# Performance work log

Hardware: AMD Instinct MI355X
Metric: run time of the kernel (lower is better)

## Reference

```python
import math
import jax, jax.numpy as jnp
import numpy as np


def setup_inputs() -> dict:
    key = jax.random.key(0)
    k1, k2, k3, k4 = jax.random.split(key, 4)
    B, CK, CV, T, H, W = 4, 64, 512, 8, 30, 30
    mk = jax.random.normal(k1, (B, CK, T, H, W), dtype=jnp.float32)
    qk = jax.random.normal(k2, (B, CK, H, W), dtype=jnp.float32)
    mv = jax.random.normal(k3, (B, CV, T, H, W), dtype=jnp.float32)
    qv = jax.random.normal(k4, (B, CV, H, W), dtype=jnp.float32)
    return {"mk": mk, "qk": qk, "mv": mv, "qv": qv}


def reference(mk, qk, mv, qv):
    # mk: [B, CK, T, H, W], qk: [B, CK, H, W]
    # mv: [B, CV, T, H, W], qv: [B, CV, H, W]
    B, CK, T, H, W = mk.shape
    CV = mv.shape[1]
    mkf = mk.reshape(B, CK, T * H * W)          # [B, CK, THW]
    qkf = qk.reshape(B, CK, H * W)              # [B, CK, HW]
    # distance-based affinity: (2 a.b - |a|^2) / sqrt(CK)
    a_sq = jnp.sum(mkf * mkf, axis=1)[:, :, None]        # [B, THW, 1]
    ab = jnp.einsum('bcm,bcq->bmq', mkf, qkf)            # [B, THW, HW]
    affinity = (2.0 * ab - a_sq) * (1.0 / math.sqrt(CK))
    # softmax over the memory dimension (THW)
    affinity = jax.nn.softmax(affinity, axis=1)          # [B, THW, HW]
    # value readout
    mvf = mv.reshape(B, CV, T * H * W)                   # [B, CV, THW]
    mem = jnp.einsum('bcm,bmq->bcq', mvf, affinity)      # [B, CV, HW]
    mem = mem.reshape(B, CV, H, W)
    return jnp.concatenate([mem, qv], axis=1)            # [B, 2*CV, H, W]
```

## Files before the change

kernel.cpp:

```cpp
#include <hip/hip_runtime.h>

#define B_ 4
#define CK 64
#define CV 512
#define HW_ 900
#define THW 7200
#define MT 96
#define QB 64
#define CVB 128
#define NS 3
#define MSPL (THW / NS)
#define NIT (MSPL / MT)
#define ETP 104

typedef __attribute__((ext_vector_type(4))) float f32x4;
typedef __attribute__((ext_vector_type(4))) float float4_;
typedef __attribute__((ext_vector_type(8))) short s16x8;
typedef __attribute__((ext_vector_type(4))) short s16x4;

__device__ __forceinline__ short f2bf(float f) {
  union { float f; unsigned u; } x; x.f = f;
  unsigned u = x.u;
  return (short)((u + 0x7fffu + ((u >> 16) & 1u)) >> 16);
}

#define NBLK_A 113
#define NBLK_B 900
#define NBLK_C 14400
#define NBLK_D 1800
__global__ __launch_bounds__(256) void prep_kernel(const float* __restrict__ mk,
                                                   const float* __restrict__ qk,
                                                   const float* __restrict__ mv,
                                                   const float* __restrict__ qv,
                                                   short* __restrict__ mkT,
                                                   short* __restrict__ qkb,
                                                   short* __restrict__ mvb,
                                                   float* __restrict__ asq,
                                                   float* __restrict__ out) {
  int bid = blockIdx.x;
  if (bid < NBLK_A) {
    int idx = bid * 256 + threadIdx.x;
    if (idx >= B_ * THW) return;
    int b = idx / THW, m = idx - b * THW;
    const float* src = mk + (size_t)b * CK * THW + m;
    short row[CK];
    float acc = 0.f;
#pragma unroll
    for (int k = 0; k < CK; ++k) {
      float v = src[(size_t)k * THW];
      acc += v * v;
      row[k] = f2bf(v);
    }
    short* dst = mkT + (size_t)idx * CK;
#pragma unroll
    for (int c = 0; c < CK / 8; ++c)
      *reinterpret_cast<s16x8*>(dst + c * 8) = *reinterpret_cast<s16x8*>(row + c * 8);
    asq[idx] = acc * 0.18033688011112042f;
  } else if (bid < NBLK_A + NBLK_B) {
    int i = (bid - NBLK_A) * 256 + threadIdx.x;
    if (i < B_ * CK * HW_) qkb[i] = f2bf(qk[i] * 0.36067376022224085f);
  } else if (bid < NBLK_A + NBLK_B + NBLK_C) {
    int i = (bid - (NBLK_A + NBLK_B)) * 256 + threadIdx.x;
    float4_ v = reinterpret_cast<const float4_*>(mv)[i];
    s16x4 o;
    o[0] = f2bf(v[0]); o[1] = f2bf(v[1]); o[2] = f2bf(v[2]); o[3] = f2bf(v[3]);
    *reinterpret_cast<s16x4*>(mvb + (size_t)i * 4) = o;
  } else {
    int i = (bid - (NBLK_A + NBLK_B + NBLK_C)) * 256 + threadIdx.x;
    const int perb = CV * HW_ / 4;
    int b = i / perb, r = i - b * perb;
    float4_ v = reinterpret_cast<const float4_*>(qv)[i];
    *reinterpret_cast<float4_*>(out + (size_t)b * 2 * CV * HW_ + CV * HW_ + (size_t)r * 4) = v;
  }
}

__global__ __launch_bounds__(256, 4) void attn_kernel(const short* __restrict__ mkT,
                                                      const short* __restrict__ qkb,
                                                      const short* __restrict__ mvb,
                                                      const float* __restrict__ asq,
                                                      float* __restrict__ part,
                                                      float* __restrict__ denomp) {
  __shared__ short e_t[64][ETP];

  const int tid = threadIdx.x;
  const int wave = tid >> 6, lane = tid & 63;
  const int g = lane >> 4, c = lane & 15;
  const int qb = blockIdx.x;
  const int cvc = blockIdx.y & 3, s = blockIdx.y >> 2;
  const int b = blockIdx.z;
  const int q = qb * QB + wave * 16 + c;

  s16x8 qkf[2];
  {
    const short* qs = qkb + (size_t)b * CK * HW_;
#pragma unroll
    for (int ks = 0; ks < 2; ++ks)
#pragma unroll
      for (int j = 0; j < 8; ++j)
        qkf[ks][j] = (q < HW_) ? qs[(size_t)(ks * 32 + g * 8 + j) * HW_ + q] : (short)0;
  }

  f32x4 acc[2][4];
#pragma unroll
  for (int i = 0; i < 2; ++i)
#pragma unroll
    for (int j = 0; j < 4; ++j) acc[i][j] = (f32x4){0.f, 0.f, 0.f, 0.f};
  float denom = 0.f;

  const short* mkb = mkT + (size_t)b * THW * CK;
  const short* mvB = mvb + ((size_t)b * CV + cvc * CVB + wave * 32) * THW;
  const float* asb = asq + (size_t)b * THW;

  for (int it = 0; it < NIT; ++it) {
    const int m0 = s * MSPL + it * MT;

    s16x8 mvf[2][3];
#pragma unroll
    for (int af = 0; af < 2; ++af)
#pragma unroll
      for (int ks = 0; ks < 3; ++ks)
        mvf[af][ks] = *reinterpret_cast<const s16x8*>(
            mvB + (size_t)(af * 16 + c) * THW + m0 + ks * 32 + g * 8);

#pragma unroll
    for (int mf = 0; mf < 6; ++mf) {
      f32x4 sa = (f32x4){0.f, 0.f, 0.f, 0.f};
#pragma unroll
      for (int ks = 0; ks < 2; ++ks) {
        s16x8 a = *reinterpret_cast<const s16x8*>(
            mkb + (size_t)(m0 + mf * 16 + c) * CK + ks * 32 + g * 8);
        sa = __builtin_amdgcn_mfma_f32_16x16x32_bf16(a, qkf[ks], sa, 0, 0, 0);
      }
      f32x4 av = *reinterpret_cast<const f32x4*>(asb + m0 + mf * 16 + g * 4);
      s16x4 e4;
#pragma unroll
      for (int r = 0; r < 4; ++r) {
        float e = exp2f(sa[r] - av[r]);
        denom += e;
        union { float f; unsigned u; } cu; cu.f = e;
        e4[r] = (short)(cu.u >> 16);
      }
      *reinterpret_cast<s16x4*>(&e_t[wave * 16 + c][mf * 16 + g * 4]) = e4;
    }
    __syncthreads();

#pragma unroll
    for (int ks = 0; ks < 3; ++ks) {
      s16x8 ef[4];
#pragma unroll
      for (int qf = 0; qf < 4; ++qf)
        ef[qf] = *reinterpret_cast<const s16x8*>(&e_t[qf * 16 + c][ks * 32 + g * 8]);
#pragma unroll
      for (int af = 0; af < 2; ++af)
#pragma unroll
        for (int qf = 0; qf < 4; ++qf)
          acc[af][qf] =
              __builtin_amdgcn_mfma_f32_16x16x32_bf16(mvf[af][ks], ef[qf], acc[af][qf], 0, 0, 0);
    }
    __syncthreads();
  }

  denom += __shfl_xor(denom, 16);
  denom += __shfl_xor(denom, 32);
  if (cvc == 0 && lane < 16)
    denomp[((size_t)s * B_ + b) * 960 + qb * QB + wave * 16 + lane] = denom;

  float* pb = part + (size_t)(((s * B_ + b) * 4 + cvc) * 15 + qb) * 8192;
#pragma unroll
  for (int af = 0; af < 2; ++af)
#pragma unroll
    for (int qf = 0; qf < 4; ++qf)
#pragma unroll
      for (int r = 0; r < 4; ++r)
        pb[(size_t)(wave * 32 + af * 16 + g * 4 + r) * 64 + qf * 16 + c] = acc[af][qf][r];
}

__global__ __launch_bounds__(256) void finalize_kernel(const float* __restrict__ part,
                                                       const float* __restrict__ denomp,
                                                       float* __restrict__ out) {
  int t = blockIdx.x * 256 + threadIdx.x;
  int q4 = t & 15;
  int cvl = (t >> 4) & 127;
  int r1 = t >> 11;
  int qb = r1 % 15;
  int r2 = r1 / 15;
  int cvc = r2 & 3;
  int b = r2 >> 2;
  int q0 = qb * QB + q4 * 4;
  if (q0 >= HW_) return;
  const size_t sstr = (size_t)B_ * 4 * 15 * 8192;
  size_t base = (size_t)((b * 4 + cvc) * 15 + qb) * 8192 + cvl * 64 + q4 * 4;
  f32x4 p = *reinterpret_cast<const f32x4*>(part + base);
  f32x4 p1 = *reinterpret_cast<const f32x4*>(part + base + sstr);
  f32x4 p2 = *reinterpret_cast<const f32x4*>(part + base + 2 * sstr);
  p = p + p1 + p2;
  const float* dp = denomp + (size_t)b * 960 + q0;
  f32x4 d = *reinterpret_cast<const f32x4*>(dp) +
            *reinterpret_cast<const f32x4*>(dp + B_ * 960) +
            *reinterpret_cast<const f32x4*>(dp + 2 * B_ * 960);
  f32x4 o;
#pragma unroll
  for (int j = 0; j < 4; ++j) o[j] = p[j] / d[j];
  *reinterpret_cast<f32x4*>(out + (size_t)b * 2 * CV * HW_ +
                            (size_t)(cvc * CVB + cvl) * HW_ + q0) = o;
}

extern "C" void kernel_launch(void* const* d_in, const int* in_sizes, int n_in,
                              void* d_out, int out_size, void* d_ws, size_t ws_size,
                              hipStream_t stream) {
  const float* mk = (const float*)d_in[0];
  const float* qk = (const float*)d_in[1];
  const float* mv = (const float*)d_in[2];
  const float* qv = (const float*)d_in[3];
  float* out = (float*)d_out;

  char* ws = (char*)d_ws;
  short* mvb   = (short*)ws;
  short* mkT   = (short*)(ws + 29491200);
  short* qkb   = (short*)(ws + 33177600);
  float* asq   = (float*)(ws + 33638400);
  float* denomp= (float*)(ws + 33753600);
  float* part  = (float*)(ws + 33799680);

  prep_kernel<<<dim3(NBLK_A + NBLK_B + NBLK_C + NBLK_D), dim3(256), 0, stream>>>(
      mk, qk, mv, qv, mkT, qkb, mvb, asq, out);
  attn_kernel<<<dim3(15, 4 * NS, B_), dim3(256), 0, stream>>>(mkT, qkb, mvb, asq, part, denomp);
  finalize_kernel<<<dim3(1920), dim3(256), 0, stream>>>(part, denomp, out);
}
```

Before: 284.6 us.

## Double-buffer mv/mk tiles into LDS via async global_load_lds with swizzling

The attention kernel now stages the value, key and asq tiles for the next memory chunk into double-buffered LDS using direct global-to-LDS loads, overlapping the fetch with compute on the current chunk. XOR swizzles are applied to avoid bank conflicts. Work is repartitioned so each wave owns 16 queries across all 128 value channels, which removes one of the two barriers per iteration. LDS use grows to roughly 90KB per block and launch bounds drop to one block per SM, which cuts occupancy and could reduce latency hiding.

```diff
diff --git a/kernel.cpp b/kernel.cpp
--- a/kernel.cpp
+++ b/kernel.cpp
@@ -11,12 +11,20 @@
 #define NS 3
 #define MSPL (THW / NS)
 #define NIT (MSPL / MT)
-#define ETP 104
 
 typedef __attribute__((ext_vector_type(4))) float f32x4;
 typedef __attribute__((ext_vector_type(4))) float float4_;
 typedef __attribute__((ext_vector_type(8))) short s16x8;
 typedef __attribute__((ext_vector_type(4))) short s16x4;
+
+#define AS1 __attribute__((address_space(1)))
+#define AS3 __attribute__((address_space(3)))
+__device__ __forceinline__ void g2l16(const void* g, void* l) {
+  __builtin_amdgcn_global_load_lds((const AS1 void*)g, (AS3 void*)l, 16, 0, 0);
+}
+__device__ __forceinline__ void g2l4(const void* g, void* l) {
+  __builtin_amdgcn_global_load_lds((const AS1 void*)g, (AS3 void*)l, 4, 0, 0);
+}
 
 __device__ __forceinline__ short f2bf(float f) {
   union { float f; unsigned u; } x; x.f = f;
@@ -74,13 +82,16 @@
   }
 }
 
-__global__ __launch_bounds__(256, 4) void attn_kernel(const short* __restrict__ mkT,
+__global__ __launch_bounds__(256, 1) void attn_kernel(const short* __restrict__ mkT,
                                                       const short* __restrict__ qkb,
                                                       const short* __restrict__ mvb,
                                                       const float* __restrict__ asq,
                                                       float* __restrict__ part,
                                                       float* __restrict__ denomp) {
-  __shared__ short e_t[64][ETP];
+  __shared__ __align__(16) short mvt[2][CVB][128];
+  __shared__ __align__(16) short mkt[2][MT][64];
+  __shared__ __align__(16) short et[4][16][128];
+  __shared__ __align__(16) float asqt[2][MT];
 
   const int tid = threadIdx.x;
   const int wave = tid >> 6, lane = tid & 63;
@@ -90,6 +101,10 @@
   const int b = blockIdx.z;
   const int q = qb * QB + wave * 16 + c;
 
+  const short* mkb = mkT + (size_t)b * THW * CK;
+  const short* mvsrc = mvb + ((size_t)b * CV + cvc * CVB) * THW;
+  const float* asb = asq + (size_t)b * THW;
+
   s16x8 qkf[2];
   {
     const short* qs = qkb + (size_t)b * CK * HW_;
@@ -100,38 +115,47 @@
         qkf[ks][j] = (q < HW_) ? qs[(size_t)(ks * 32 + g * 8 + j) * HW_ + q] : (short)0;
   }
 
-  f32x4 acc[2][4];
-#pragma unroll
-  for (int i = 0; i < 2; ++i)
-#pragma unroll
-    for (int j = 0; j < 4; ++j) acc[i][j] = (f32x4){0.f, 0.f, 0.f, 0.f};
+  f32x4 acc[8];
+#pragma unroll
+  for (int i = 0; i < 8; ++i) acc[i] = (f32x4){0.f, 0.f, 0.f, 0.f};
   float denom = 0.f;
 
-  const short* mkb = mkT + (size_t)b * THW * CK;
-  const short* mvB = mvb + ((size_t)b * CV + cvc * CVB + wave * 32) * THW;
-  const float* asb = asq + (size_t)b * THW;
+  auto STAGE = [&](int t, int nb) {
+    const int m0 = s * MSPL + t * MT;
+#pragma unroll
+    for (int p = 0; p < 8; ++p) {
+      int ch = p * 256 + tid;
+      int row = ch >> 4, sl = ch & 15;
+      int so = (sl * 16) ^ ((row & 15) << 4);
+      g2l16(mvsrc + (size_t)row * THW + m0 + (so >> 1), (short*)mvt[nb] + ch * 8);
+    }
+#pragma unroll
+    for (int p = 0; p < 3; ++p) {
+      int ch = p * 256 + tid;
+      int row = ch >> 3, sl = ch & 7;
+      int so = (sl * 16) ^ ((row & 7) << 4);
+      g2l16(mkb + (size_t)(m0 + row) * CK + (so >> 1), (short*)mkt[nb] + ch * 8);
+    }
+    if (tid < MT) g2l4(asb + m0 + tid, &asqt[nb][tid]);
+  };
+
+  STAGE(0, 0);
+  __syncthreads();
 
   for (int it = 0; it < NIT; ++it) {
-    const int m0 = s * MSPL + it * MT;
-
-    s16x8 mvf[2][3];
-#pragma unroll
-    for (int af = 0; af < 2; ++af)
-#pragma unroll
-      for (int ks = 0; ks < 3; ++ks)
-        mvf[af][ks] = *reinterpret_cast<const s16x8*>(
-            mvB + (size_t)(af * 16 + c) * THW + m0 + ks * 32 + g * 8);
+    const int pb = it & 1, nb = pb ^ 1;
+    if (it + 1 < NIT) STAGE(it + 1, nb);
 
 #pragma unroll
     for (int mf = 0; mf < 6; ++mf) {
       f32x4 sa = (f32x4){0.f, 0.f, 0.f, 0.f};
 #pragma unroll
       for (int ks = 0; ks < 2; ++ks) {
-        s16x8 a = *reinterpret_cast<const s16x8*>(
-            mkb + (size_t)(m0 + mf * 16 + c) * CK + ks * 32 + g * 8);
+        int cb = (ks * 64 + g * 16) ^ ((c & 7) << 4);
+        s16x8 a = *reinterpret_cast<const s16x8*>(&mkt[pb][mf * 16 + c][cb >> 1]);
         sa = __builtin_amdgcn_mfma_f32_16x16x32_bf16(a, qkf[ks], sa, 0, 0, 0);
       }
-      f32x4 av = *reinterpret_cast<const f32x4*>(asb + m0 + mf * 16 + g * 4);
+      f32x4 av = *reinterpret_cast<const f32x4*>(&asqt[pb][mf * 16 + g * 4]);
       s16x4 e4;
 #pragma unroll
       for (int r = 0; r < 4; ++r) {
@@ -140,22 +164,19 @@
         union { float f; unsigned u; } cu; cu.f = e;
         e4[r] = (short)(cu.u >> 16);
       }
-      *reinterpret_cast<s16x4*>(&e_t[wave * 16 + c][mf * 16 + g * 4]) = e4;
-    }
-    __syncthreads();
+      int cbw = ((mf * 32 + g * 8) ^ ((c & 15) << 4)) >> 1;
+      *reinterpret_cast<s16x4*>(&et[wave][c][cbw]) = e4;
+    }
 
 #pragma unroll
     for (int ks = 0; ks < 3; ++ks) {
-      s16x8 ef[4];
-#pragma unroll
-      for (int qf = 0; qf < 4; ++qf)
-        ef[qf] = *reinterpret_cast<const s16x8*>(&e_t[qf * 16 + c][ks * 32 + g * 8]);
-#pragma unroll
-      for (int af = 0; af < 2; ++af)
-#pragma unroll
-        for (int qf = 0; qf < 4; ++qf)
-          acc[af][qf] =
-              __builtin_amdgcn_mfma_f32_16x16x32_bf16(mvf[af][ks], ef[qf], acc[af][qf], 0, 0, 0);
+      int cb = ((ks * 64 + g * 16) ^ ((c & 15) << 4)) >> 1;
+      s16x8 bfr = *reinterpret_cast<const s16x8*>(&et[wave][c][cb]);
+#pragma unroll
+      for (int cf = 0; cf < 8; ++cf) {
+        s16x8 afr = *reinterpret_cast<const s16x8*>(&mvt[pb][cf * 16 + c][cb]);
+        acc[cf] = __builtin_amdgcn_mfma_f32_16x16x32_bf16(afr, bfr, acc[cf], 0, 0, 0);
+      }
     }
     __syncthreads();
   }
@@ -165,14 +186,12 @@
   if (cvc == 0 && lane < 16)
     denomp[((size_t)s * B_ + b) * 960 + qb * QB + wave * 16 + lane] = denom;
 
-  float* pb = part + (size_t)(((s * B_ + b) * 4 + cvc) * 15 + qb) * 8192;
-#pragma unroll
-  for (int af = 0; af < 2; ++af)
-#pragma unroll
-    for (int qf = 0; qf < 4; ++qf)
-#pragma unroll
-      for (int r = 0; r < 4; ++r)
-        pb[(size_t)(wave * 32 + af * 16 + g * 4 + r) * 64 + qf * 16 + c] = acc[af][qf][r];
+  float* pb0 = part + (size_t)(((s * B_ + b) * 4 + cvc) * 15 + qb) * 8192 + wave * 16 + c;
+#pragma unroll
+  for (int cf = 0; cf < 8; ++cf)
+#pragma unroll
+    for (int r = 0; r < 4; ++r)
+      pb0[(size_t)(cf * 16 + g * 4 + r) * 64] = acc[cf][r];
 }
 
 __global__ __launch_bounds__(256) void finalize_kernel(const float* __restrict__ part,
```

Result: faster. 261.2 us (-8.2%).
